# Kernel optimization log

Hardware: AMD Instinct MI355X
Metric: run time of the kernel (lower is better)

Reference implementation:

```python
import jax, jax.numpy as jnp
import numpy as np

MARGIN = 1.25

N, D = 262144, 128

def setup_inputs() -> dict:
    key = jax.random.key(0)
    k1, k2, k3 = jax.random.split(key, 3)
    output1 = jax.random.normal(k1, (N, D), dtype=jnp.float32)
    output2 = jax.random.normal(k2, (N, D), dtype=jnp.float32)
    desire = jax.random.uniform(k3, (N, 1), dtype=jnp.float32)
    return {"output1": output1, "output2": output2, "desire": desire}

def reference(output1, output2, desire):
    margin = MARGIN / 2.0  # 0.625
    # Per-row euclidean distance (the torch loop recomputes this identical
    # vector length times; computing it once is the same math).
    diff = output1 - output2                      # [N, D]
    dist = jnp.sqrt(jnp.sum(diff * diff, axis=1))  # [N]
    actual = (dist > margin).astype(jnp.float32)[:, None]  # [N, 1]
    intersection = jnp.sum(actual * desire)
    union = jnp.sum(actual) + jnp.sum(desire) - intersection
    return (intersection + 1e-06) / (union + 1e-06)
```

## Files before the change

kernel.cpp:

```cpp
#include <hip/hip_runtime.h>

#define NROWS   262144
#define DCOLS   128
#define NBLOCKS 2048
#define MARGIN_SQ 0.390625f

typedef float v4f __attribute__((ext_vector_type(4)));

__global__ __launch_bounds__(256) void fra_main(const float* __restrict__ o1,
                                                const float* __restrict__ o2,
                                                const float* __restrict__ desire,
                                                float* __restrict__ ws) {
    __shared__ float s_inter[4], s_act[4], s_des[4];
    const int tid  = threadIdx.x;
    const int lane = tid & 63;
    const int wave = tid >> 6;
    const int h    = lane >> 5;
    const int wgid = blockIdx.x * 4 + wave;
    const int r0   = wgid * 32;

    float l_inter = 0.0f, l_act = 0.0f, l_des = 0.0f;

    #pragma unroll
    for (int p = 0; p < 16; p++) {
        const int rp = r0 + 2 * p;
        const v4f* __restrict__ a = (const v4f*)(o1 + (size_t)rp * DCOLS);
        const v4f* __restrict__ b = (const v4f*)(o2 + (size_t)rp * DCOLS);

        const float d = desire[rp + h];

        const v4f va = __builtin_nontemporal_load(&a[lane]);
        const v4f vb = __builtin_nontemporal_load(&b[lane]);

        const v4f df = va - vb;
        float s = df.x * df.x + df.y * df.y + df.z * df.z + df.w * df.w;

        s += __shfl_xor(s, 1);
        s += __shfl_xor(s, 2);
        s += __shfl_xor(s, 4);
        s += __shfl_xor(s, 8);
        s += __shfl_xor(s, 16);

        const float act = (s > MARGIN_SQ) ? 1.0f : 0.0f;
        l_act   += act;
        l_des   += d;
        l_inter += act * d;
    }

    #pragma unroll
    for (int off = 1; off <= 32; off <<= 1) {
        l_inter += __shfl_xor(l_inter, off);
        l_act   += __shfl_xor(l_act,   off);
        l_des   += __shfl_xor(l_des,   off);
    }

    if (lane == 0) {
        s_inter[wave] = l_inter * 0.03125f;
        s_act[wave]   = l_act   * 0.03125f;
        s_des[wave]   = l_des   * 0.03125f;
    }
    __syncthreads();
    if (tid == 0) {
        ws[blockIdx.x]               = s_inter[0] + s_inter[1] + s_inter[2] + s_inter[3];
        ws[NBLOCKS + blockIdx.x]     = s_act[0]   + s_act[1]   + s_act[2]   + s_act[3];
        ws[2 * NBLOCKS + blockIdx.x] = s_des[0]   + s_des[1]   + s_des[2]   + s_des[3];
    }
}

__global__ __launch_bounds__(1024) void fra_reduce(const float* __restrict__ ws,
                                                   float* __restrict__ out) {
    __shared__ float s[3][16];
    const int t = threadIdx.x;
    float i = ws[t]        + ws[t + 1024];
    float a = ws[2048 + t] + ws[2048 + t + 1024];
    float d = ws[4096 + t] + ws[4096 + t + 1024];

    #pragma unroll
    for (int off = 32; off >= 1; off >>= 1) {
        i += __shfl_xor(i, off);
        a += __shfl_xor(a, off);
        d += __shfl_xor(d, off);
    }
    const int lane = t & 63, w = t >> 6;
    if (lane == 0) { s[0][w] = i; s[1][w] = a; s[2][w] = d; }
    __syncthreads();
    if (t == 0) {
        float ti = 0.0f, ta = 0.0f, td = 0.0f;
        #pragma unroll
        for (int k = 0; k < 16; k++) { ti += s[0][k]; ta += s[1][k]; td += s[2][k]; }
        const float uni = ta + td - ti;
        out[0] = (ti + 1e-6f) / (uni + 1e-6f);
    }
}

extern "C" void kernel_launch(void* const* d_in, const int* in_sizes, int n_in,
                              void* d_out, int out_size, void* d_ws, size_t ws_size,
                              hipStream_t stream) {
    const float* o1     = (const float*)d_in[0];
    const float* o2     = (const float*)d_in[1];
    const float* desire = (const float*)d_in[2];
    float*       out    = (float*)d_out;
    float*       ws     = (float*)d_ws;

    fra_main<<<NBLOCKS, 256, 0, stream>>>(o1, o2, desire, ws);
    fra_reduce<<<1, 1024, 0, stream>>>(ws, out);
}
```

Before: 252.2 us.

## Double-buffer row loads in groups and load desire once per wave

Result: no change. 252.6 us (+0.1%).

```diff
diff --git a/kernel.cpp b/kernel.cpp
--- a/kernel.cpp
+++ b/kernel.cpp
@@ -6,6 +6,35 @@
 #define MARGIN_SQ 0.390625f
 
 typedef float v4f __attribute__((ext_vector_type(4)));
+
+
+#define LOADB(da, db, pb)                                                   \
+  {                                                                         \
+    _Pragma("unroll")                                                       \
+    for (int k = 0; k < 4; k++) {                                           \
+      da[k] = __builtin_nontemporal_load(&a[((pb) * 4 + k) * 64 + lane]);   \
+      db[k] = __builtin_nontemporal_load(&b[((pb) * 4 + k) * 64 + lane]);   \
+    }                                                                       \
+  }
+
+#define COMPB(sa, sb, pb)                                                   \
+  {                                                                         \
+    _Pragma("unroll")                                                       \
+    for (int k = 0; k < 4; k++) {                                           \
+      const int p = (pb) * 4 + k;                                           \
+      const v4f df = sa[k] - sb[k];                                         \
+      float s = df.x * df.x + df.y * df.y + df.z * df.z + df.w * df.w;      \
+      s += __shfl_xor(s, 1);                                                \
+      s += __shfl_xor(s, 2);                                                \
+      s += __shfl_xor(s, 4);                                                \
+      s += __shfl_xor(s, 8);                                                \
+      s += __shfl_xor(s, 16);                                               \
+      const float act = (s > MARGIN_SQ) ? 1.0f : 0.0f;                      \
+      const float sel = ((lane & 31) == 2 * p + h) ? 1.0f : 0.0f;           \
+      l_act   += act * sel;                                                 \
+      l_inter += act * dv * sel;                                            \
+    }                                                                       \
+  }
 
 __global__ __launch_bounds__(256) void fra_main(const float* __restrict__ o1,
                                                 const float* __restrict__ o2,
@@ -19,34 +48,26 @@
     const int wgid = blockIdx.x * 4 + wave;
     const int r0   = wgid * 32;
 
-    float l_inter = 0.0f, l_act = 0.0f, l_des = 0.0f;
+    const v4f* __restrict__ a = (const v4f*)(o1 + (size_t)r0 * DCOLS);
+    const v4f* __restrict__ b = (const v4f*)(o2 + (size_t)r0 * DCOLS);
 
-    #pragma unroll
-    for (int p = 0; p < 16; p++) {
-        const int rp = r0 + 2 * p;
-        const v4f* __restrict__ a = (const v4f*)(o1 + (size_t)rp * DCOLS);
-        const v4f* __restrict__ b = (const v4f*)(o2 + (size_t)rp * DCOLS);
+    const float dv = desire[r0 + (lane & 31)];
 
-        const float d = desire[rp + h];
+    float l_inter = 0.0f, l_act = 0.0f;
 
-        const v4f va = __builtin_nontemporal_load(&a[lane]);
-        const v4f vb = __builtin_nontemporal_load(&b[lane]);
+    v4f vaA[4], vbA[4], vaB[4], vbB[4];
 
-        const v4f df = va - vb;
-        float s = df.x * df.x + df.y * df.y + df.z * df.z + df.w * df.w;
+    LOADB(vaA, vbA, 0);
+    LOADB(vaB, vbB, 1);
 
-        s += __shfl_xor(s, 1);
-        s += __shfl_xor(s, 2);
-        s += __shfl_xor(s, 4);
-        s += __shfl_xor(s, 8);
-        s += __shfl_xor(s, 16);
+    COMPB(vaA, vbA, 0);
+    LOADB(vaA, vbA, 2);
+    COMPB(vaB, vbB, 1);
+    LOADB(vaB, vbB, 3);
+    COMPB(vaA, vbA, 2);
+    COMPB(vaB, vbB, 3);
 
-        const float act = (s > MARGIN_SQ) ? 1.0f : 0.0f;
-        l_act   += act;
-        l_des   += d;
-        l_inter += act * d;
-    }
-
+    float l_des = dv;
     #pragma unroll
     for (int off = 1; off <= 32; off <<= 1) {
         l_inter += __shfl_xor(l_inter, off);
@@ -55,9 +76,9 @@
     }
 
     if (lane == 0) {
-        s_inter[wave] = l_inter * 0.03125f;
-        s_act[wave]   = l_act   * 0.03125f;
-        s_des[wave]   = l_des   * 0.03125f;
+        s_inter[wave] = l_inter;
+        s_act[wave]   = l_act;
+        s_des[wave]   = l_des * 0.5f;
     }
     __syncthreads();
     if (tid == 0) {
```
